# Optimization experiments

Hardware: AMD Instinct MI355X
Metric: run time of the kernel (lower is better)

The kernel has to match this reference:

```python
import jax, jax.numpy as jnp
import numpy as np

B, T, C, H, U = 16, 2048, 512, 4, 250
L, R = 1, 1              # l_order, r_order -> depthwise kernel size 3
K = L + R + 1
SMOOTH, NOISE = 1.0, 0.0  # smooth_factor, noise_threshold


def setup_inputs() -> dict:
    key = jax.random.key(0)
    k0, k1, k2, k3 = jax.random.split(key, 4)
    hidden = jax.random.normal(k0, (B, T, C), dtype=jnp.float32)
    mask = jnp.ones((B, 1, T), dtype=jnp.float32)
    target_label_length = jax.random.randint(k1, (B,), 0, U).astype(jnp.int32)
    # parameters
    conv_w = jax.random.normal(k2, (C, 1, K), dtype=jnp.float32) / np.sqrt(K)   # depthwise Conv1d weight [O, I/g=1, K]
    conv_b = jnp.zeros((C,), dtype=jnp.float32)
    lin_w = jax.random.normal(k3, (1, C), dtype=jnp.float32) / np.sqrt(C)       # cif_output Linear(idim, 1)
    lin_b = jnp.zeros((1,), dtype=jnp.float32)
    sigma = jnp.full((H,), 0.5, dtype=jnp.float32)
    sigma_bias = jnp.zeros((H,), dtype=jnp.float32)
    return {
        "hidden": hidden, "mask": mask, "target_label_length": target_label_length,
        "max_token": U, "conv_w": conv_w, "conv_b": conv_b,
        "lin_w": lin_w, "lin_b": lin_b, "sigma": sigma, "sigma_bias": sigma_bias,
    }


def reference(hidden, mask, target_label_length, max_token, conv_w, conv_b, lin_w, lin_b, sigma, sigma_bias):
    b, t, c = hidden.shape
    h = sigma.shape[0]
    # --- alpha prediction branch ---
    context = jnp.swapaxes(hidden, 1, 2)                       # [B, C, T]
    queries = jnp.pad(context, ((0, 0), (0, 0), (L, R)))       # ConstantPad1d((l, r), 0)
    memory = jax.lax.conv_general_dilated(
        queries, conv_w, window_strides=(1,), padding='VALID',
        feature_group_count=c, dimension_numbers=('NCH', 'OIH', 'NCH'))
    memory = memory + conv_b[None, :, None]
    out = jnp.swapaxes(memory + context, 1, 2)                 # [B, T, C]  (dropout = identity in eval)
    out = jax.nn.relu(out)
    out = out @ lin_w.T + lin_b                                # [B, T, 1]
    alphas = jax.nn.relu(jax.nn.sigmoid(out) * SMOOTH - NOISE)
    mask_bt1 = jnp.swapaxes(mask, -1, -2)                      # [B, T, 1]
    alphas = (alphas * mask_bt1)[..., 0]                       # [B, T]
    mask_bt = mask_bt1[..., 0]                                 # [B, T]
    # --- CIF scaling to target length ---
    target_length = target_label_length.astype(jnp.float32)   # [B]
    token_num = alphas.sum(-1)                                 # [B] (pre-scaling, as in torch)
    alphas = alphas * (target_length / token_num)[:, None]
    alignment = jnp.cumsum(alphas, axis=-1)                    # [B, T]
    # --- Gaussian soft-segment attention ---
    fire_positions = jnp.arange(max_token, dtype=alphas.dtype) + 0.5            # [U]
    dist = fire_positions[None, None, :, None] - alignment[:, None, None, :]    # [B, 1, U, T]
    scores = -(dist * sigma[None, :, None, None]) ** 2 + sigma_bias[None, :, None, None]  # [B, H, U, T]
    scores = jnp.where(mask_bt[:, None, None, :] > 0, scores, -jnp.inf)
    weights = jax.nn.softmax(scores, axis=-1)                  # [B, H, U, T]
    n_hidden = hidden.reshape(b, t, h, c // h).transpose(0, 2, 1, 3)            # [B, H, T, Dh]
    acoustic = jnp.einsum('bhut,bhtd->bhud', weights, n_hidden)                 # [B, H, U, Dh]
    acoustic_embeds = acoustic.transpose(0, 2, 1, 3).reshape(b, max_token, c)   # [B, U, C]
    return acoustic_embeds, token_num, alphas
```

## Files before the change

### kernel.cpp

```cpp
#include <hip/hip_runtime.h>

namespace {
constexpr int kB = 16, kT = 2048, kC = 512, kH = 4, kU = 250, kDH = 128;
constexpr int kTW = 32;
constexpr int kNTB = kT / kTW;
}

typedef __attribute__((ext_vector_type(8))) short short8;
typedef __attribute__((ext_vector_type(4))) float float4v;

__device__ __forceinline__ unsigned int pk_bf16(float lo, float hi) {
    unsigned int r;
    asm volatile("v_cvt_pk_bf16_f32 %0, %1, %2" : "=v"(r) : "v"(lo), "v"(hi));
    return r;
}
__device__ __forceinline__ float exp2_fast(float x) {
    float r;
    asm volatile("v_exp_f32 %0, %1" : "=v"(r) : "v"(x));
    return r;
}

__global__ __launch_bounds__(256) void k1_alpha(
    const float* __restrict__ hid, const float* __restrict__ mask,
    const float* __restrict__ conv_w, const float* __restrict__ conv_b,
    const float* __restrict__ lin_w, const float* __restrict__ lin_b,
    float* __restrict__ alpha_raw, unsigned short* __restrict__ Vt)
{
    __shared__ float halo[4][2][512];
    const int wave = threadIdx.x >> 6, lane = threadIdx.x & 63;
    const int b = blockIdx.x >> 6;
    const int tb = blockIdx.x & 63;
    const int tblk = tb << 5;
    const int t0 = tblk + wave * 8;
    const int c0 = lane * 8;

    float cw[24], cb[8], lw[8];
    #pragma unroll
    for (int i = 0; i < 6; i++) *(float4*)&cw[i*4] = ((const float4*)(conv_w + c0*3))[i];
    *(float4*)&cb[0] = *(const float4*)(conv_b + c0);
    *(float4*)&cb[4] = *(const float4*)(conv_b + c0 + 4);
    *(float4*)&lw[0] = *(const float4*)(lin_w + c0);
    *(float4*)&lw[4] = *(const float4*)(lin_w + c0 + 4);
    const float lb = lin_b[0];

    float r[10][8];
    const float* base = hid + ((size_t)b * kT + t0) * kC + c0;
    #pragma unroll
    for (int i = 1; i <= 8; i++) {
        const float* p = base + (ptrdiff_t)(i - 1) * kC;
        *(float4*)&r[i][0] = *(const float4*)p;
        *(float4*)&r[i][4] = *(const float4*)(p + 4);
    }
    *(float4*)&halo[wave][0][c0]     = *(float4*)&r[1][0];
    *(float4*)&halo[wave][0][c0 + 4] = *(float4*)&r[1][4];
    *(float4*)&halo[wave][1][c0]     = *(float4*)&r[8][0];
    *(float4*)&halo[wave][1][c0 + 4] = *(float4*)&r[8][4];

    if (wave == 0) {
        if (tblk > 0) {
            const float* p = base - kC;
            *(float4*)&r[0][0] = *(const float4*)p;
            *(float4*)&r[0][4] = *(const float4*)(p + 4);
        } else {
            #pragma unroll
            for (int j = 0; j < 8; j++) r[0][j] = 0.f;
        }
    }
    if (wave == 3) {
        if (tblk + 32 < kT) {
            const float* p = base + 8 * kC;
            *(float4*)&r[9][0] = *(const float4*)p;
            *(float4*)&r[9][4] = *(const float4*)(p + 4);
        } else {
            #pragma unroll
            for (int j = 0; j < 8; j++) r[9][j] = 0.f;
        }
    }

    {
        unsigned short* tile = Vt + (size_t)(b * kNTB + tb) * kC * kTW;
        #pragma unroll
        for (int e = 0; e < 8; e++) {
            unsigned int vw[4];
            vw[0] = pk_bf16(r[1][e], r[2][e]);
            vw[1] = pk_bf16(r[3][e], r[4][e]);
            vw[2] = pk_bf16(r[5][e], r[6][e]);
            vw[3] = pk_bf16(r[7][e], r[8][e]);
            *(uint4*)(tile + (c0 + e) * kTW + wave * 8) = *(const uint4*)vw;
        }
    }

    __syncthreads();
    if (wave > 0) {
        *(float4*)&r[0][0] = *(float4*)&halo[wave - 1][1][c0];
        *(float4*)&r[0][4] = *(float4*)&halo[wave - 1][1][c0 + 4];
    }
    if (wave < 3) {
        *(float4*)&r[9][0] = *(float4*)&halo[wave + 1][0][c0];
        *(float4*)&r[9][4] = *(float4*)&halo[wave + 1][0][c0 + 4];
    }

    float sums[8];
    #pragma unroll
    for (int j = 0; j < 8; j++) {
        float acc = 0.f;
        #pragma unroll
        for (int k = 0; k < 8; k++) {
            float m = fmaf(r[j][k], cw[k*3],
                      fmaf(r[j+1][k], cw[k*3+1],
                      fmaf(r[j+2][k], cw[k*3+2], cb[k])));
            float v = m + r[j+1][k];
            v = v > 0.f ? v : 0.f;
            acc = fmaf(v, lw[k], acc);
        }
        #pragma unroll
        for (int off = 32; off >= 1; off >>= 1) acc += __shfl_xor(acc, off, 64);
        sums[j] = acc;
    }
    if (lane == 0) {
        #pragma unroll
        for (int j = 0; j < 8; j++) {
            float s = sums[j] + lb;
            float a = 1.f / (1.f + expf(-s));
            alpha_raw[(size_t)b * kT + t0 + j] = a * mask[(size_t)b * kT + t0 + j];
        }
    }
}

__global__ __launch_bounds__(256) void k2_scan(
    const float* __restrict__ alpha_raw, const float* __restrict__ mask,
    const int* __restrict__ target,
    float* __restrict__ al, float* __restrict__ out_tok, float* __restrict__ out_alpha)
{
    __shared__ float woff[4];
    __shared__ float s_tot;
    const int b = blockIdx.x, tid = threadIdx.x;
    const int wave = tid >> 6, lane = tid & 63;

    float a[8], m[8];
    const float* ar = alpha_raw + (size_t)b * kT + tid * 8;
    const float* mr = mask + (size_t)b * kT + tid * 8;
    *(float4*)&a[0] = *(const float4*)ar;
    *(float4*)&a[4] = *(const float4*)(ar + 4);
    *(float4*)&m[0] = *(const float4*)mr;
    *(float4*)&m[4] = *(const float4*)(mr + 4);

    float pre[8]; float run = 0.f;
    #pragma unroll
    for (int j = 0; j < 8; j++) { run += a[j]; pre[j] = run; }
    float sc = run;
    #pragma unroll
    for (int off = 1; off <= 32; off <<= 1) {
        float v = __shfl_up(sc, off, 64);
        sc = (lane >= off) ? sc + v : sc;
    }
    if (lane == 63) woff[wave] = sc;
    __syncthreads();
    if (tid == 0) {
        float r2 = 0.f;
        #pragma unroll
        for (int w = 0; w < 4; w++) { float x = woff[w]; woff[w] = r2; r2 += x; }
        s_tot = r2;
    }
    __syncthreads();
    const float tot = s_tot;
    const float scale = (tot != 0.f) ? ((float)target[b] / tot) : 0.f;
    const float basev = woff[wave] + (sc - run);

    float alv[8], oav[8];
    #pragma unroll
    for (int j = 0; j < 8; j++) {
        alv[j] = (m[j] > 0.f) ? (basev + pre[j]) * scale : 1.0e30f;
        oav[j] = a[j] * scale;
    }
    float* alw = al + (size_t)b * kT + tid * 8;
    float* oaw = out_alpha + (size_t)b * kT + tid * 8;
    *(float4*)alw       = *(const float4*)&alv[0];
    *(float4*)(alw + 4) = *(const float4*)&alv[4];
    *(float4*)oaw       = *(const float4*)&oav[0];
    *(float4*)(oaw + 4) = *(const float4*)&oav[4];
    if (tid == 0) out_tok[b] = tot;
}

__global__ __launch_bounds__(256, 4) void k3_attn(
    const unsigned short* __restrict__ Vt, const float* __restrict__ al,
    const float* __restrict__ sigma, float* __restrict__ out_ac)
{
    __shared__ float al_s[kT];

    const int ut = blockIdx.x, h = blockIdx.y, b = blockIdx.z;
    const int tid = threadIdx.x;
    const int wave = tid >> 6, lane = tid & 63;
    const int lm = lane & 15, quad = lane >> 4;
    const int u0 = ut * 16;
    const int cb = h * kDH + wave * 32;
    const float sig = sigma[h];
    const float sigL = sig * 1.2011224f;

    {
        const float4* alg = (const float4*)(al + (size_t)b * kT);
        ((float4*)al_s)[tid]       = alg[tid];
        ((float4*)al_s)[tid + 256] = alg[tid + 256];
    }
    __syncthreads();

    const float du = (float)(u0 + lm) + 0.5f;
    const float duL = du * sigL;
    int pos = 0;
    #pragma unroll
    for (int stp = 1024; stp >= 1; stp >>= 1) {
        int np = pos + stp;
        pos = (al_s[np - 1] < du) ? np : pos;
    }
    float d1 = (pos < kT) ? al_s[pos] - du : 3.0e30f;
    float d0 = (pos > 0) ? du - al_s[pos - 1] : 3.0e30f;
    float dmin = fminf(d0, d1);
    float dmn = fminf(dmin, 1.0e4f);
    float ms = dmn * sigL;
    const float mu_pos = ms * ms;

    const float c21 = (sig > 1e-3f) ? 21.0f / (sig * sig) : 9.0e60f;
    const float bnd = sqrtf(fmaf(dmn, dmn, c21));
    float lo_l = du - bnd, hi_l = du + bnd;
    #pragma unroll
    for (int off = 8; off >= 1; off >>= 1) {
        lo_l = fminf(lo_l, __shfl_xor(lo_l, off, 64));
        hi_l = fmaxf(hi_l, __shfl_xor(hi_l, off, 64));
    }
    int p_lo = 0, p_hi = 0;
    #pragma unroll
    for (int stp = 1024; stp >= 1; stp >>= 1) {
        int n1 = p_lo + stp; p_lo = (al_s[n1 - 1] < lo_l) ? n1 : p_lo;
        int n2 = p_hi + stp; p_hi = (al_s[n2 - 1] < hi_l) ? n2 : p_hi;
    }
    const int ks_lo = p_lo >> 5;
    const int ks_end = (p_hi + 31) >> 5;

    float4v acc0 = (float4v)(0.f), acc1 = (float4v)(0.f);
    float lsum = 0.f;

    const unsigned short* vbase = Vt + (size_t)b * kNTB * kC * kTW
                                     + (cb + lm) * kTW + quad * 8;

    #pragma unroll 4
    for (int kg = ks_lo; kg < ks_end; kg++) {
        const int kb = kg * kTW;
        float alv[8];
        *(float4*)&alv[0] = *(const float4*)&al_s[kb + quad * 8];
        *(float4*)&alv[4] = *(const float4*)&al_s[kb + quad * 8 + 4];

        float ev[8];
        #pragma unroll
        for (int j = 0; j < 8; j++) {
            float d = fmaf(-alv[j], sigL, duL);
            float e = exp2_fast(fmaf(-d, d, mu_pos));
            lsum += e;
            ev[j] = e;
        }
        union { short8 s; unsigned int w[4]; } af;
        af.w[0] = pk_bf16(ev[0], ev[1]);
        af.w[1] = pk_bf16(ev[2], ev[3]);
        af.w[2] = pk_bf16(ev[4], ev[5]);
        af.w[3] = pk_bf16(ev[6], ev[7]);

        const unsigned short* vp = vbase + (size_t)kg * kC * kTW;
        short8 bf0 = *(const short8*)(vp);
        short8 bf1 = *(const short8*)(vp + 16 * kTW);
        acc0 = __builtin_amdgcn_mfma_f32_16x16x32_bf16(af.s, bf0, acc0, 0, 0, 0);
        acc1 = __builtin_amdgcn_mfma_f32_16x16x32_bf16(af.s, bf1, acc1, 0, 0, 0);
    }

    float lv = lsum;
    lv += __shfl_xor(lv, 16, 64);
    lv += __shfl_xor(lv, 32, 64);
    #pragma unroll
    for (int r = 0; r < 4; r++) {
        const int ur = quad * 4 + r;
        float rl = __shfl(lv, ur, 64);
        float linv = (rl > 1e-30f) ? 1.f / rl : 0.f;
        const int u = u0 + ur;
        if (u < kU) {
            float* dst = out_ac + ((size_t)(b * kU + u)) * kC + cb + lm;
            dst[0]  = acc0[r] * linv;
            dst[16] = acc1[r] * linv;
        }
    }
}

extern "C" void kernel_launch(void* const* d_in, const int* in_sizes, int n_in,
                              void* d_out, int out_size, void* d_ws, size_t ws_size,
                              hipStream_t stream) {
    const float* hid    = (const float*)d_in[0];
    const float* mask   = (const float*)d_in[1];
    const int*   tgt    = (const int*)d_in[2];
    const float* conv_w = (const float*)d_in[4];
    const float* conv_b = (const float*)d_in[5];
    const float* lin_w  = (const float*)d_in[6];
    const float* lin_b  = (const float*)d_in[7];
    const float* sigma  = (const float*)d_in[8];

    float* alpha_raw = (float*)d_ws;
    float* al        = (float*)((char*)d_ws + 131072);
    unsigned short* Vt = (unsigned short*)((char*)d_ws + 262144);

    float* out_ac    = (float*)d_out;
    float* out_tok   = out_ac + (size_t)kB * kU * kC;
    float* out_alpha = out_tok + kB;

    k1_alpha<<<kB * kT / 32, 256, 0, stream>>>(hid, mask, conv_w, conv_b, lin_w, lin_b,
                                               alpha_raw, Vt);
    k2_scan<<<kB, 256, 0, stream>>>(alpha_raw, mask, tgt, al, out_tok, out_alpha);
    k3_attn<<<dim3(16, kH, kB), 256, 0, stream>>>(Vt, al, sigma, out_ac);
}
```

Baseline: 157.6 us.

## Store bf16 V row-major and transpose in-kernel via shuffles and LDS

k1 now writes the bf16 copy of hidden in natural [B,T,C] layout with contiguous 16-byte stores per row, replacing the strided transposed-tile writes. k3 loads 32-bit pairs from the row-major layout, recombines them with cross-lane shuffles, stages a per-wave transposed tile in LDS, and reads MFMA B operands from there. It also flattens the grid to 1D with a remapped block order that interleaves u-tiles. The change cuts the cost of k1's scattered stores but adds shuffles, LDS traffic and narrower strided global loads in the attention inner loop, and drops that loop's unroll pragma.

```diff
diff --git a/kernel.cpp b/kernel.cpp
--- a/kernel.cpp
+++ b/kernel.cpp
@@ -3,7 +3,6 @@
 namespace {
 constexpr int kB = 16, kT = 2048, kC = 512, kH = 4, kU = 250, kDH = 128;
 constexpr int kTW = 32;
-constexpr int kNTB = kT / kTW;
 }
 
 typedef __attribute__((ext_vector_type(8))) short short8;
@@ -24,13 +23,12 @@
     const float* __restrict__ hid, const float* __restrict__ mask,
     const float* __restrict__ conv_w, const float* __restrict__ conv_b,
     const float* __restrict__ lin_w, const float* __restrict__ lin_b,
-    float* __restrict__ alpha_raw, unsigned short* __restrict__ Vt)
+    float* __restrict__ alpha_raw, unsigned short* __restrict__ Vn)
 {
     __shared__ float halo[4][2][512];
     const int wave = threadIdx.x >> 6, lane = threadIdx.x & 63;
     const int b = blockIdx.x >> 6;
-    const int tb = blockIdx.x & 63;
-    const int tblk = tb << 5;
+    const int tblk = (blockIdx.x & 63) << 5;
     const int t0 = tblk + wave * 8;
     const int c0 = lane * 8;
 
@@ -51,6 +49,16 @@
         *(float4*)&r[i][0] = *(const float4*)p;
         *(float4*)&r[i][4] = *(const float4*)(p + 4);
     }
+    #pragma unroll
+    for (int j = 1; j <= 8; j++) {
+        unsigned int vw[4];
+        vw[0] = pk_bf16(r[j][0], r[j][1]);
+        vw[1] = pk_bf16(r[j][2], r[j][3]);
+        vw[2] = pk_bf16(r[j][4], r[j][5]);
+        vw[3] = pk_bf16(r[j][6], r[j][7]);
+        *(uint4*)(Vn + ((size_t)b * kT + t0 + j - 1) * kC + c0) = *(const uint4*)vw;
+    }
+
     *(float4*)&halo[wave][0][c0]     = *(float4*)&r[1][0];
     *(float4*)&halo[wave][0][c0 + 4] = *(float4*)&r[1][4];
     *(float4*)&halo[wave][1][c0]     = *(float4*)&r[8][0];
@@ -76,20 +84,6 @@
             for (int j = 0; j < 8; j++) r[9][j] = 0.f;
         }
     }
-
-    {
-        unsigned short* tile = Vt + (size_t)(b * kNTB + tb) * kC * kTW;
-        #pragma unroll
-        for (int e = 0; e < 8; e++) {
-            unsigned int vw[4];
-            vw[0] = pk_bf16(r[1][e], r[2][e]);
-            vw[1] = pk_bf16(r[3][e], r[4][e]);
-            vw[2] = pk_bf16(r[5][e], r[6][e]);
-            vw[3] = pk_bf16(r[7][e], r[8][e]);
-            *(uint4*)(tile + (c0 + e) * kTW + wave * 8) = *(const uint4*)vw;
-        }
-    }
-
     __syncthreads();
     if (wave > 0) {
         *(float4*)&r[0][0] = *(float4*)&halo[wave - 1][1][c0];
@@ -183,12 +177,16 @@
 }
 
 __global__ __launch_bounds__(256, 4) void k3_attn(
-    const unsigned short* __restrict__ Vt, const float* __restrict__ al,
+    const unsigned short* __restrict__ Vn, const float* __restrict__ al,
     const float* __restrict__ sigma, float* __restrict__ out_ac)
 {
     __shared__ float al_s[kT];
-
-    const int ut = blockIdx.x, h = blockIdx.y, b = blockIdx.z;
+    __shared__ unsigned short vt[4][32][40];
+
+    const int i = blockIdx.x;
+    const int bh = i >> 4, m = (i >> 3) & 1, x = i & 7;
+    const int ut = 2 * x + m;
+    const int b = bh >> 2, h = bh & 3;
     const int tid = threadIdx.x;
     const int wave = tid >> 6, lane = tid & 63;
     const int lm = lane & 15, quad = lane >> 4;
@@ -239,20 +237,25 @@
     float4v acc0 = (float4v)(0.f), acc1 = (float4v)(0.f);
     float lsum = 0.f;
 
-    const unsigned short* vbase = Vt + (size_t)b * kNTB * kC * kTW
-                                     + (cb + lm) * kTW + quad * 8;
-
-    #pragma unroll 4
+    const int c2l = (lm) * 2;
+    const int trow = quad;
+    const unsigned short* vsrc = Vn + (size_t)b * kT * kC + cb + c2l;
+
     for (int kg = ks_lo; kg < ks_end; kg++) {
         const int kb = kg * kTW;
-        float alv[8];
-        *(float4*)&alv[0] = *(const float4*)&al_s[kb + quad * 8];
-        *(float4*)&alv[4] = *(const float4*)&al_s[kb + quad * 8 + 4];
-
+
+        unsigned int vv[8];
+        #pragma unroll
+        for (int ip = 0; ip < 8; ip++)
+            vv[ip] = *(const unsigned int*)(vsrc + (size_t)(kb + ip * 4 + trow) * kC);
+
+        float alvv[8];
+        *(float4*)&alvv[0] = *(const float4*)&al_s[kb + quad * 8];
+        *(float4*)&alvv[4] = *(const float4*)&al_s[kb + quad * 8 + 4];
         float ev[8];
         #pragma unroll
         for (int j = 0; j < 8; j++) {
-            float d = fmaf(-alv[j], sigL, duL);
+            float d = fmaf(-alvv[j], sigL, duL);
             float e = exp2_fast(fmaf(-d, d, mu_pos));
             lsum += e;
             ev[j] = e;
@@ -263,9 +266,24 @@
         af.w[2] = pk_bf16(ev[4], ev[5]);
         af.w[3] = pk_bf16(ev[6], ev[7]);
 
-        const unsigned short* vp = vbase + (size_t)kg * kC * kTW;
-        short8 bf0 = *(const short8*)(vp);
-        short8 bf1 = *(const short8*)(vp + 16 * kTW);
+        #pragma unroll
+        for (int ip = 0; ip < 8; ip++) {
+            unsigned int v = vv[ip];
+            unsigned int p = (unsigned int)__shfl_xor((int)v, 16, 64);
+            const int tp = ip * 2 + (trow >> 1);
+            unsigned int w; int c_w;
+            if ((trow & 1) == 0) {
+                w = (v & 0xffffu) | (p << 16);
+                c_w = c2l;
+            } else {
+                w = (p >> 16) | (v & 0xffff0000u);
+                c_w = c2l + 1;
+            }
+            *(unsigned int*)&vt[wave][c_w][tp * 2] = w;
+        }
+
+        short8 bf0 = *(const short8*)&vt[wave][lm][quad * 8];
+        short8 bf1 = *(const short8*)&vt[wave][lm + 16][quad * 8];
         acc0 = __builtin_amdgcn_mfma_f32_16x16x32_bf16(af.s, bf0, acc0, 0, 0, 0);
         acc1 = __builtin_amdgcn_mfma_f32_16x16x32_bf16(af.s, bf1, acc1, 0, 0, 0);
     }
@@ -301,14 +319,14 @@
 
     float* alpha_raw = (float*)d_ws;
     float* al        = (float*)((char*)d_ws + 131072);
-    unsigned short* Vt = (unsigned short*)((char*)d_ws + 262144);
+    unsigned short* Vn = (unsigned short*)((char*)d_ws + 262144);
 
     float* out_ac    = (float*)d_out;
     float* out_tok   = out_ac + (size_t)kB * kU * kC;
     float* out_alpha = out_tok + kB;
 
     k1_alpha<<<kB * kT / 32, 256, 0, stream>>>(hid, mask, conv_w, conv_b, lin_w, lin_b,
-                                               alpha_raw, Vt);
+                                               alpha_raw, Vn);
     k2_scan<<<kB, 256, 0, stream>>>(alpha_raw, mask, tgt, al, out_tok, out_alpha);
-    k3_attn<<<dim3(16, kH, kB), 256, 0, stream>>>(Vt, al, sigma, out_ac);
-}
+    k3_attn<<<1024, 256, 0, stream>>>(Vn, al, sigma, out_ac);
+}
```

Result: slower. 171.2 us (+8.6%).

## Drop bf16 transposed V copy and read fp32 hidden directly in attention

Applied to the files above, without the earlier changes.

The alpha kernel no longer writes a transposed bf16 copy of hidden. The attention kernel instead loads fp32 hidden values straight from global memory in strided per-row scalar loads and converts them to bf16 in registers before the MFMA. This removes a 16 MB write and the later re-read of the tile layout. The cost is uncoalesced-ish 4-byte loads with a 2 KB stride, twice the bytes per element, and extra conversion work. The inline asm helpers also lose their volatile qualifier, so the compiler can schedule them freely.

```diff
diff --git a/kernel.cpp b/kernel.cpp
--- a/kernel.cpp
+++ b/kernel.cpp
@@ -3,7 +3,6 @@
 namespace {
 constexpr int kB = 16, kT = 2048, kC = 512, kH = 4, kU = 250, kDH = 128;
 constexpr int kTW = 32;
-constexpr int kNTB = kT / kTW;
 }
 
 typedef __attribute__((ext_vector_type(8))) short short8;
@@ -11,12 +10,12 @@
 
 __device__ __forceinline__ unsigned int pk_bf16(float lo, float hi) {
     unsigned int r;
-    asm volatile("v_cvt_pk_bf16_f32 %0, %1, %2" : "=v"(r) : "v"(lo), "v"(hi));
+    asm("v_cvt_pk_bf16_f32 %0, %1, %2" : "=v"(r) : "v"(lo), "v"(hi));
     return r;
 }
 __device__ __forceinline__ float exp2_fast(float x) {
     float r;
-    asm volatile("v_exp_f32 %0, %1" : "=v"(r) : "v"(x));
+    asm("v_exp_f32 %0, %1" : "=v"(r) : "v"(x));
     return r;
 }
 
@@ -24,13 +23,12 @@
     const float* __restrict__ hid, const float* __restrict__ mask,
     const float* __restrict__ conv_w, const float* __restrict__ conv_b,
     const float* __restrict__ lin_w, const float* __restrict__ lin_b,
-    float* __restrict__ alpha_raw, unsigned short* __restrict__ Vt)
+    float* __restrict__ alpha_raw)
 {
     __shared__ float halo[4][2][512];
     const int wave = threadIdx.x >> 6, lane = threadIdx.x & 63;
     const int b = blockIdx.x >> 6;
-    const int tb = blockIdx.x & 63;
-    const int tblk = tb << 5;
+    const int tblk = (blockIdx.x & 63) << 5;
     const int t0 = tblk + wave * 8;
     const int c0 = lane * 8;
 
@@ -76,20 +74,6 @@
             for (int j = 0; j < 8; j++) r[9][j] = 0.f;
         }
     }
-
-    {
-        unsigned short* tile = Vt + (size_t)(b * kNTB + tb) * kC * kTW;
-        #pragma unroll
-        for (int e = 0; e < 8; e++) {
-            unsigned int vw[4];
-            vw[0] = pk_bf16(r[1][e], r[2][e]);
-            vw[1] = pk_bf16(r[3][e], r[4][e]);
-            vw[2] = pk_bf16(r[5][e], r[6][e]);
-            vw[3] = pk_bf16(r[7][e], r[8][e]);
-            *(uint4*)(tile + (c0 + e) * kTW + wave * 8) = *(const uint4*)vw;
-        }
-    }
-
     __syncthreads();
     if (wave > 0) {
         *(float4*)&r[0][0] = *(float4*)&halo[wave - 1][1][c0];
@@ -183,7 +167,7 @@
 }
 
 __global__ __launch_bounds__(256, 4) void k3_attn(
-    const unsigned short* __restrict__ Vt, const float* __restrict__ al,
+    const float* __restrict__ hid, const float* __restrict__ al,
     const float* __restrict__ sigma, float* __restrict__ out_ac)
 {
     __shared__ float al_s[kT];
@@ -239,35 +223,45 @@
     float4v acc0 = (float4v)(0.f), acc1 = (float4v)(0.f);
     float lsum = 0.f;
 
-    const unsigned short* vbase = Vt + (size_t)b * kNTB * kC * kTW
-                                     + (cb + lm) * kTW + quad * 8;
-
-    #pragma unroll 4
+    const float* vcol0 = hid + (size_t)b * kT * kC + cb + lm;
+    const float* vcol1 = vcol0 + 16;
+
+    #pragma unroll 2
     for (int kg = ks_lo; kg < ks_end; kg++) {
         const int kb = kg * kTW;
-        float alv[8];
-        *(float4*)&alv[0] = *(const float4*)&al_s[kb + quad * 8];
-        *(float4*)&alv[4] = *(const float4*)&al_s[kb + quad * 8 + 4];
-
+        const int tb0 = kb + quad * 8;
+
+        float v0[8], v1[8];
+        #pragma unroll
+        for (int j = 0; j < 8; j++) {
+            v0[j] = vcol0[(size_t)(tb0 + j) * kC];
+            v1[j] = vcol1[(size_t)(tb0 + j) * kC];
+        }
+
+        float alvv[8];
+        *(float4*)&alvv[0] = *(const float4*)&al_s[kb + quad * 8];
+        *(float4*)&alvv[4] = *(const float4*)&al_s[kb + quad * 8 + 4];
         float ev[8];
         #pragma unroll
         for (int j = 0; j < 8; j++) {
-            float d = fmaf(-alv[j], sigL, duL);
+            float d = fmaf(-alvv[j], sigL, duL);
             float e = exp2_fast(fmaf(-d, d, mu_pos));
             lsum += e;
             ev[j] = e;
         }
-        union { short8 s; unsigned int w[4]; } af;
+        union { short8 s; unsigned int w[4]; } af, bf0, bf1;
         af.w[0] = pk_bf16(ev[0], ev[1]);
         af.w[1] = pk_bf16(ev[2], ev[3]);
         af.w[2] = pk_bf16(ev[4], ev[5]);
         af.w[3] = pk_bf16(ev[6], ev[7]);
 
-        const unsigned short* vp = vbase + (size_t)kg * kC * kTW;
-        short8 bf0 = *(const short8*)(vp);
-        short8 bf1 = *(const short8*)(vp + 16 * kTW);
-        acc0 = __builtin_amdgcn_mfma_f32_16x16x32_bf16(af.s, bf0, acc0, 0, 0, 0);
-        acc1 = __builtin_amdgcn_mfma_f32_16x16x32_bf16(af.s, bf1, acc1, 0, 0, 0);
+        #pragma unroll
+        for (int p2 = 0; p2 < 4; p2++) {
+            bf0.w[p2] = pk_bf16(v0[2*p2], v0[2*p2 + 1]);
+            bf1.w[p2] = pk_bf16(v1[2*p2], v1[2*p2 + 1]);
+        }
+        acc0 = __builtin_amdgcn_mfma_f32_16x16x32_bf16(af.s, bf0.s, acc0, 0, 0, 0);
+        acc1 = __builtin_amdgcn_mfma_f32_16x16x32_bf16(af.s, bf1.s, acc1, 0, 0, 0);
     }
 
     float lv = lsum;
@@ -301,14 +295,13 @@
 
     float* alpha_raw = (float*)d_ws;
     float* al        = (float*)((char*)d_ws + 131072);
-    unsigned short* Vt = (unsigned short*)((char*)d_ws + 262144);
 
     float* out_ac    = (float*)d_out;
     float* out_tok   = out_ac + (size_t)kB * kU * kC;
     float* out_alpha = out_tok + kB;
 
     k1_alpha<<<kB * kT / 32, 256, 0, stream>>>(hid, mask, conv_w, conv_b, lin_w, lin_b,
-                                               alpha_raw, Vt);
+                                               alpha_raw);
     k2_scan<<<kB, 256, 0, stream>>>(alpha_raw, mask, tgt, al, out_tok, out_alpha);
-    k3_attn<<<dim3(16, kH, kB), 256, 0, stream>>>(Vt, al, sigma, out_ac);
-}
+    k3_attn<<<dim3(16, kH, kB), 256, 0, stream>>>(hid, al, sigma, out_ac);
+}
```

New measurement: 157.3 us. No clear change (-0.2%).
